# Performance work log

Measured on AMD Instinct MI355X. Metric: run time of the kernel, lower is better.

The kernel has to match this reference:

```python
import jax, jax.numpy as jnp
import numpy as np

N_NODES = 50000
N_EDGES = 800000
D = 128  # in_dim == hidden_dim


def setup_inputs() -> dict:
    key = jax.random.key(0)
    k1, k2, k3, k4 = jax.random.split(key, 4)
    x = jax.random.normal(k1, (N_NODES, D), dtype=jnp.float32)
    edge_index = jax.random.randint(k2, (2, N_EDGES), 0, N_NODES, dtype=jnp.int64)
    # Glorot-ish scale for square weights
    scale = 1.0 / np.sqrt(D)
    W1 = jax.random.normal(k3, (D, D), dtype=jnp.float32) * scale
    W2 = jax.random.normal(k4, (D, D), dtype=jnp.float32) * scale
    b1 = jnp.zeros((D,), dtype=jnp.float32)
    b2 = jnp.zeros((D,), dtype=jnp.float32)
    return {"x": x, "edge_index": edge_index, "W1": W1, "b1": b1, "W2": W2, "b2": b2}


def _gcn_layer(x, W, b, src, dst, norm, n):
    # PyG GCNConv: h = x @ W, then symmetric-normalized scatter-add, then + bias
    h = x @ W                                   # [N, D] dense GEMM
    msg = h[src] * norm[:, None]                # [E', D] gather + scale
    out = jax.ops.segment_sum(msg, dst, num_segments=n)  # scatter-add
    return out + b


def reference(x, edge_index, W1, b1, W2, b2):
    n = x.shape[0]
    # add self-loops (GCNConv default add_self_loops=True)
    loops = jnp.arange(n, dtype=edge_index.dtype)
    src = jnp.concatenate([edge_index[0], loops])
    dst = jnp.concatenate([edge_index[1], loops])
    # symmetric normalization: deg^{-1/2}[src] * deg^{-1/2}[dst]
    deg = jax.ops.segment_sum(jnp.ones_like(src, dtype=x.dtype), dst, num_segments=n)
    dinv = jax.lax.rsqrt(jnp.maximum(deg, 1.0))  # deg >= 1 due to self-loops
    norm = dinv[src] * dinv[dst]
    # layer 1: conv -> relu (dropout is identity in eval mode)
    h = jax.nn.relu(_gcn_layer(x, W1, b1, src, dst, norm, n))
    # layer 2 (cut='c2'): conv -> relu
    h = jax.nn.relu(_gcn_layer(h, W2, b2, src, dst, norm, n))
    return h
```

## Files before the change

### kernel.cpp

```cpp
#include <hip/hip_runtime.h>
#include <hip/hip_fp16.h>

#define NN 50000
#define NE 800000
#define DD 128
#define NSTRIP 3125
#define NB 196
#define CHUNK 4096
#define MAXB 6144

#define OF_LCNT  0
#define OF_LOFS  50176
#define OF_DINV  100352
#define OF_DEG   150352
#define OF_OFFS2 200352
#define OF_TMP2  300352
#define OF_CSRW  1103168
#define OF_H1    2307392
#define OF_H2    5507392
#define OF_W1H   8707392
#define OF_W1L   8715584
#define OF_W2H   8723776
#define OF_W2L   8731968

typedef __attribute__((ext_vector_type(8))) short bf8_t;
typedef __attribute__((ext_vector_type(8))) unsigned short us8;
typedef __attribute__((ext_vector_type(4))) float f32x4;

static __device__ __forceinline__ unsigned short f2bf(float f) {
    unsigned int u = __float_as_uint(f);
    unsigned int r = (u + 0x7fffu + ((u >> 16) & 1u)) >> 16;
    return (unsigned short)r;
}
static __device__ __forceinline__ float bf2f(unsigned short h) {
    return __uint_as_float(((unsigned int)h) << 16);
}

__global__ void k_wconv(const float* __restrict__ W1, const float* __restrict__ W2,
                        ushort* __restrict__ w1h, ushort* __restrict__ w1l,
                        ushort* __restrict__ w2h, ushort* __restrict__ w2l,
                        int* __restrict__ deg) {
    int gg = blockIdx.x * 256 + threadIdx.x;
    for (int i = gg; i < NN; i += 4096) deg[i] = 0;
    const float* W = (gg < 2048) ? W1 : W2;
    ushort* wh = (gg < 2048) ? w1h : w2h;
    ushort* wl = (gg < 2048) ? w1l : w2l;
    int g = gg & 2047;
    int ntile = g >> 8;
    int kk = (g >> 6) & 3;
    int lane = g & 63;
    int k0 = kk * 32 + ((lane >> 4) * 8);
    int col = ntile * 16 + (lane & 15);
#pragma unroll
    for (int j = 0; j < 8; ++j) {
        float w = W[(k0 + j) * DD + col];
        unsigned short h = f2bf(w);
        wh[(size_t)g * 8 + j] = h;
        wl[(size_t)g * 8 + j] = f2bf(w - bf2f(h));
    }
}

__global__ __launch_bounds__(256) void k_prep(
        const int* __restrict__ src, const int* __restrict__ dst,
        int* __restrict__ lcnt_g, int* __restrict__ lofs_g,
        unsigned int* __restrict__ tmp2, int* __restrict__ deg,
        const float* __restrict__ X,
        const ushort* __restrict__ wh, const ushort* __restrict__ wl,
        ushort* __restrict__ H1) {
    __shared__ int lcnt[256];
    __shared__ int lsc[256];
    __shared__ int lcur[256];
    int tid = threadIdx.x;
    if (blockIdx.x < 196) {
        int blk = blockIdx.x;
        lcnt[tid] = 0;
        __syncthreads();
        int e0 = blk * CHUNK;
        int e1 = e0 + CHUNK; if (e1 > NE) e1 = NE;
        for (int e = e0 + tid; e < e1; e += 256) {
            int d = dst[e];
            atomicAdd(&lcnt[d >> 8], 1);
            atomicAdd(&deg[d], 1);
        }
        __syncthreads();
        int v = lcnt[tid];
        lsc[tid] = v;
        __syncthreads();
        for (int o = 1; o < 256; o <<= 1) {
            int t = (tid >= o) ? lsc[tid - o] : 0;
            __syncthreads();
            lsc[tid] += t;
            __syncthreads();
        }
        int excl = lsc[tid] - v;
        lcnt_g[tid * 196 + blk] = v;
        lofs_g[tid * 196 + blk] = excl;
        lcur[tid] = excl;
        __syncthreads();
        for (int e = e0 + tid; e < e1; e += 256) {
            int d = dst[e], s = src[e];
            int b = d >> 8;
            int r = atomicAdd(&lcur[b], 1);
            tmp2[blk * CHUNK + r] = ((unsigned int)s << 8) | (unsigned int)(d & 255);
        }
        return;
    }
    int wave = tid >> 6;
    int lane = tid & 63;
    int strip = (blockIdx.x - 196) * 4 + wave;
    if (strip >= NSTRIP) return;
    int rb = strip << 4;
    int m = lane & 15;
    int quad = lane >> 4;
    const float* ar = X + (size_t)(rb + m) * DD;
    f32x4 acc[8];
#pragma unroll
    for (int t = 0; t < 8; ++t) acc[t] = (f32x4){0.f, 0.f, 0.f, 0.f};
#pragma unroll
    for (int kk = 0; kk < 4; ++kk) {
        float4 xa = *(const float4*)(ar + kk * 32 + quad * 8);
        float4 xb = *(const float4*)(ar + kk * 32 + quad * 8 + 4);
        float xs[8] = {xa.x, xa.y, xa.z, xa.w, xb.x, xb.y, xb.z, xb.w};
        bf8_t ah, al;
#pragma unroll
        for (int j = 0; j < 8; ++j) {
            unsigned short hh = f2bf(xs[j]);
            ah[j] = (short)hh;
            al[j] = (short)f2bf(xs[j] - bf2f(hh));
        }
#pragma unroll
        for (int t = 0; t < 8; ++t) {
            size_t bo = ((size_t)(t * 4 + kk) * 64 + lane) * 8;
            bf8_t bh = *(const bf8_t*)(wh + bo);
            bf8_t bl = *(const bf8_t*)(wl + bo);
            acc[t] = __builtin_amdgcn_mfma_f32_16x16x32_bf16(ah, bh, acc[t], 0, 0, 0);
            acc[t] = __builtin_amdgcn_mfma_f32_16x16x32_bf16(ah, bl, acc[t], 0, 0, 0);
            acc[t] = __builtin_amdgcn_mfma_f32_16x16x32_bf16(al, bh, acc[t], 0, 0, 0);
        }
    }
#pragma unroll
    for (int t = 0; t < 8; ++t) {
#pragma unroll
        for (int r = 0; r < 4; ++r)
            H1[(size_t)(rb + quad * 4 + r) * DD + t * 16 + m] = f2bf(acc[t][r]);
    }
}

__global__ __launch_bounds__(256) void k_sort(const int* __restrict__ lcnt_g,
                                              const int* __restrict__ lofs_g,
                                              const unsigned int* __restrict__ tmp2,
                                              const int* __restrict__ deg,
                                              unsigned int* __restrict__ csrw,
                                              int2* __restrict__ offs2,
                                              float* __restrict__ dinv) {
    __shared__ unsigned int ent[MAXB];
    __shared__ int c[256];
    __shared__ int p[256];
    __shared__ int o[256];
    __shared__ int cnt[256];
    __shared__ int boff[256];
    __shared__ int cur[256];
    __shared__ float sdv[256];
    int b = blockIdx.x, tid = threadIdx.x;
    int cv = (tid < 196) ? lcnt_g[b * 196 + tid] : 0;
    o[tid] = (tid < 196) ? lofs_g[b * 196 + tid] : 0;
    c[tid] = cv;
    p[tid] = cv;
    cnt[tid] = 0;
    __syncthreads();
    for (int s = 1; s < 256; s <<= 1) {
        int t = (tid >= s) ? p[tid - s] : 0;
        __syncthreads();
        p[tid] += t;
        __syncthreads();
    }
    int nb = p[255];
    for (int i = tid; i < nb; i += 256) {
        int lo = 0, hi = 255;
#pragma unroll
        for (int it = 0; it < 8; ++it) {
            int mid = (lo + hi) >> 1;
            if (p[mid] > i) hi = mid; else lo = mid + 1;
        }
        int blk = lo;
        int j = i - (p[blk] - c[blk]);
        unsigned int e = tmp2[blk * CHUNK + o[blk] + j];
        ent[i] = e;
        atomicAdd(&cnt[e & 255], 1);
    }
    __syncthreads();
    int v = cnt[tid];
    boff[tid] = v;
    __syncthreads();
    for (int s = 1; s < 256; s <<= 1) {
        int t = (tid >= s) ? boff[tid - s] : 0;
        __syncthreads();
        boff[tid] += t;
        __syncthreads();
    }
    int excl = boff[tid] - v;
    int base = b * MAXB;
    int node = b * 256 + tid;
    float dv = rsqrtf((float)(v + 1));
    sdv[tid] = dv;
    if (node < NN) {
        offs2[node] = make_int2(base + excl, base + excl + v);
        dinv[node] = dv;
    }
    cur[tid] = excl;
    __syncthreads();
    for (int i = tid; i < nb; i += 256) {
        unsigned int e = ent[i];
        int bin = e & 255;
        int s = (int)(e >> 8);
        int r = atomicAdd(&cur[bin], 1);
        float w = rsqrtf((float)(deg[s] + 1)) * sdv[bin];
        csrw[base + r] = ((unsigned int)s << 16) |
                         (unsigned int)__half_as_ushort(__float2half(w));
    }
}

__global__ __launch_bounds__(512) void k_aggmm(const ushort* __restrict__ h1,
                                               const float* __restrict__ dinv,
                                               const int2* __restrict__ offs2,
                                               const unsigned int* __restrict__ csrw,
                                               const float* __restrict__ b1,
                                               const ushort* __restrict__ w2h,
                                               const ushort* __restrict__ w2l,
                                               ushort* __restrict__ h2) {
    __shared__ float xs[16][136];
    int wave = threadIdx.x >> 6;
    int lane = threadIdx.x & 63;
    int rb = blockIdx.x * 16;
    int q = lane >> 4;
    int l = lane & 15;
    const float* bp = b1 + 8 * l;
    for (int nn = 0; nn < 2; ++nn) {
        int node = rb + wave * 2 + nn;
        int2 oe = offs2[node];
        int e1 = oe.y;
        float a[8] = {0.f, 0.f, 0.f, 0.f, 0.f, 0.f, 0.f, 0.f};
        for (int eb = oe.x; eb < e1; eb += 32) {
            int s[8]; float w[8];
#pragma unroll
            for (int j = 0; j < 8; ++j) {
                int e = eb + q + 4 * j;
                int er = (e < e1) ? e : (e1 - 1);
                er = (er < 0) ? 0 : er;
                unsigned int rw = csrw[er];
                s[j] = (int)(rw >> 16);
                w[j] = (e < e1)
                     ? __half2float(__ushort_as_half((unsigned short)(rw & 0xffffu)))
                     : 0.f;
            }
            us8 v[8];
#pragma unroll
            for (int j = 0; j < 8; ++j)
                v[j] = *(const us8*)(h1 + ((size_t)s[j] << 7) + 8 * l);
#pragma unroll
            for (int j = 0; j < 8; ++j) {
#pragma unroll
                for (int d = 0; d < 8; ++d) a[d] += w[j] * bf2f(v[j][d]);
            }
        }
        float dnode = dinv[node];
        if (q == 0) {
            us8 v = *(const us8*)(h1 + ((size_t)node << 7) + 8 * l);
            float ws = dnode * dnode;
#pragma unroll
            for (int j = 0; j < 8; ++j) a[j] += ws * bf2f(v[j]);
        }
#pragma unroll
        for (int j = 0; j < 8; ++j) {
            a[j] += __shfl_xor(a[j], 16, 64);
            a[j] += __shfl_xor(a[j], 32, 64);
        }
        if (q == 0) {
            float* xr = &xs[wave * 2 + nn][8 * l];
#pragma unroll
            for (int j = 0; j < 8; ++j)
                xr[j] = fmaxf(a[j] + bp[j], 0.f);
        }
    }
    __syncthreads();
    int m = lane & 15;
    int quad = lane >> 4;
    int t = wave;
    f32x4 acc = (f32x4){0.f, 0.f, 0.f, 0.f};
#pragma unroll
    for (int kk = 0; kk < 4; ++kk) {
        const float* xr = &xs[m][kk * 32 + quad * 8];
        float4 xa = *(const float4*)xr;
        float4 xb = *(const float4*)(xr + 4);
        float xv[8] = {xa.x, xa.y, xa.z, xa.w, xb.x, xb.y, xb.z, xb.w};
        bf8_t ah, al;
#pragma unroll
        for (int j = 0; j < 8; ++j) {
            unsigned short hh = f2bf(xv[j]);
            ah[j] = (short)hh;
            al[j] = (short)f2bf(xv[j] - bf2f(hh));
        }
        size_t bo = ((size_t)(t * 4 + kk) * 64 + lane) * 8;
        bf8_t bh = *(const bf8_t*)(w2h + bo);
        bf8_t bl = *(const bf8_t*)(w2l + bo);
        acc = __builtin_amdgcn_mfma_f32_16x16x32_bf16(ah, bh, acc, 0, 0, 0);
        acc = __builtin_amdgcn_mfma_f32_16x16x32_bf16(ah, bl, acc, 0, 0, 0);
        acc = __builtin_amdgcn_mfma_f32_16x16x32_bf16(al, bh, acc, 0, 0, 0);
    }
#pragma unroll
    for (int r = 0; r < 4; ++r)
        h2[(size_t)(rb + quad * 4 + r) * DD + t * 16 + m] = f2bf(acc[r]);
}

__global__ __launch_bounds__(256) void k_agg(const ushort* __restrict__ h,
                                             const float* __restrict__ dinv,
                                             const int2* __restrict__ offs2,
                                             const unsigned int* __restrict__ csrw,
                                             const float* __restrict__ bias,
                                             float* __restrict__ outf) {
    int wave = threadIdx.x >> 6;
    int lane = threadIdx.x & 63;
    int node = blockIdx.x * 4 + wave;
    int q = lane >> 4;
    int l = lane & 15;
    int2 oe = offs2[node];
    int e1 = oe.y;
    float a[8] = {0.f, 0.f, 0.f, 0.f, 0.f, 0.f, 0.f, 0.f};
    for (int eb = oe.x; eb < e1; eb += 32) {
        int s[8]; float w[8];
#pragma unroll
        for (int j = 0; j < 8; ++j) {
            int e = eb + q + 4 * j;
            int er = (e < e1) ? e : (e1 - 1);
            er = (er < 0) ? 0 : er;
            unsigned int rw = csrw[er];
            s[j] = (int)(rw >> 16);
            w[j] = (e < e1)
                 ? __half2float(__ushort_as_half((unsigned short)(rw & 0xffffu)))
                 : 0.f;
        }
        us8 v[8];
#pragma unroll
        for (int j = 0; j < 8; ++j)
            v[j] = *(const us8*)(h + ((size_t)s[j] << 7) + 8 * l);
#pragma unroll
        for (int j = 0; j < 8; ++j) {
#pragma unroll
            for (int d = 0; d < 8; ++d) a[d] += w[j] * bf2f(v[j][d]);
        }
    }
    float dnode = dinv[node];
    if (q == 0) {
        us8 v = *(const us8*)(h + ((size_t)node << 7) + 8 * l);
        float ws = dnode * dnode;
#pragma unroll
        for (int j = 0; j < 8; ++j) a[j] += ws * bf2f(v[j]);
    }
#pragma unroll
    for (int j = 0; j < 8; ++j) {
        a[j] += __shfl_xor(a[j], 16, 64);
        a[j] += __shfl_xor(a[j], 32, 64);
    }
    if (q == 0) {
        float* op = outf + (size_t)node * DD + 8 * l;
        const float* bp = bias + 8 * l;
        float4 o0, o1;
        o0.x = fmaxf(a[0] + bp[0], 0.f);
        o0.y = fmaxf(a[1] + bp[1], 0.f);
        o0.z = fmaxf(a[2] + bp[2], 0.f);
        o0.w = fmaxf(a[3] + bp[3], 0.f);
        o1.x = fmaxf(a[4] + bp[4], 0.f);
        o1.y = fmaxf(a[5] + bp[5], 0.f);
        o1.z = fmaxf(a[6] + bp[6], 0.f);
        o1.w = fmaxf(a[7] + bp[7], 0.f);
        *(float4*)op = o0;
        *(float4*)(op + 4) = o1;
    }
}

extern "C" void kernel_launch(void* const* d_in, const int* in_sizes, int n_in,
                              void* d_out, int out_size, void* d_ws, size_t ws_size,
                              hipStream_t stream) {
    const float* x  = (const float*)d_in[0];
    const int*   ei = (const int*)d_in[1];
    const float* W1 = (const float*)d_in[2];
    const float* b1 = (const float*)d_in[3];
    const float* W2 = (const float*)d_in[4];
    const float* b2 = (const float*)d_in[5];
    float* out = (float*)d_out;

    const int* src = ei;
    const int* dst = ei + NE;

    int*          wsi  = (int*)d_ws;
    float*        wsf  = (float*)d_ws;
    ushort*       wsu  = (ushort*)d_ws;
    unsigned int* wsuw = (unsigned int*)d_ws;
    int*    lcnt_g = wsi + OF_LCNT;
    int*    lofs_g = wsi + OF_LOFS;
    float*  dinv   = wsf + OF_DINV;
    int*    deg    = wsi + OF_DEG;
    int2*   offs2  = (int2*)(wsi + OF_OFFS2);
    unsigned int* tmp2 = wsuw + OF_TMP2;
    unsigned int* csrw = wsuw + OF_CSRW;
    ushort* h1     = wsu + (size_t)OF_H1 * 2;
    ushort* h2     = wsu + (size_t)OF_H2 * 2;
    ushort* w1h    = wsu + (size_t)OF_W1H * 2;
    ushort* w1l    = wsu + (size_t)OF_W1L * 2;
    ushort* w2h    = wsu + (size_t)OF_W2H * 2;
    ushort* w2l    = wsu + (size_t)OF_W2L * 2;

    hipLaunchKernelGGL(k_wconv, dim3(16), dim3(256), 0, stream,
                       W1, W2, w1h, w1l, w2h, w2l, deg);
    hipLaunchKernelGGL(k_prep, dim3(196 + (NSTRIP + 3) / 4), dim3(256), 0, stream,
                       src, dst, lcnt_g, lofs_g, tmp2, deg, x, w1h, w1l, h1);
    hipLaunchKernelGGL(k_sort, dim3(NB), dim3(256), 0, stream,
                       lcnt_g, lofs_g, tmp2, deg, csrw, offs2, dinv);
    hipLaunchKernelGGL(k_aggmm, dim3(NSTRIP), dim3(512), 0, stream,
                       h1, dinv, offs2, csrw, b1, w2h, w2l, h2);
    hipLaunchKernelGGL(k_agg, dim3(NN / 4), dim3(256), 0, stream,
                       h2, dinv, offs2, csrw, b2, out);
}
```

Before: 226.7 us.

## Drop per-edge weights and global degree atomics; merge prep kernels into two launches

Removes the global degree atomic counter and the per-edge fp16 weight packing. CSR entries are now 16-bit source indices only, and aggregation fetches dinv[src] per edge and applies dinv[dst] once after summation. Weight conversion is merged with bucketing, and the first GEMM is merged with the sort kernel, going from five launches to four. The cost is an extra random dinv gather per edge during both aggregations, in exchange for less global atomic traffic, half-size CSR entries and one fewer launch.

Measured after the change: 220.3 us. 1.03x faster.

```diff
diff --git a/kernel.cpp b/kernel.cpp
--- a/kernel.cpp
+++ b/kernel.cpp
@@ -1,5 +1,4 @@
 #include <hip/hip_runtime.h>
-#include <hip/hip_fp16.h>
 
 #define NN 50000
 #define NE 800000
@@ -12,16 +11,15 @@
 #define OF_LCNT  0
 #define OF_LOFS  50176
 #define OF_DINV  100352
-#define OF_DEG   150352
-#define OF_OFFS2 200352
-#define OF_TMP2  300352
-#define OF_CSRW  1103168
-#define OF_H1    2307392
-#define OF_H2    5507392
-#define OF_W1H   8707392
-#define OF_W1L   8715584
-#define OF_W2H   8723776
-#define OF_W2L   8731968
+#define OF_OFFS2 150352
+#define OF_TMP2  250352
+#define OF_CSRU  1053168
+#define OF_H1    1655280
+#define OF_H2    4855280
+#define OF_W1H   8055280
+#define OF_W1L   8063472
+#define OF_W2H   8071664
+#define OF_W2L   8079856
 
 typedef __attribute__((ext_vector_type(8))) short bf8_t;
 typedef __attribute__((ext_vector_type(8))) unsigned short us8;
@@ -36,72 +34,135 @@
     return __uint_as_float(((unsigned int)h) << 16);
 }
 
-__global__ void k_wconv(const float* __restrict__ W1, const float* __restrict__ W2,
-                        ushort* __restrict__ w1h, ushort* __restrict__ w1l,
-                        ushort* __restrict__ w2h, ushort* __restrict__ w2l,
-                        int* __restrict__ deg) {
-    int gg = blockIdx.x * 256 + threadIdx.x;
-    for (int i = gg; i < NN; i += 4096) deg[i] = 0;
-    const float* W = (gg < 2048) ? W1 : W2;
-    ushort* wh = (gg < 2048) ? w1h : w2h;
-    ushort* wl = (gg < 2048) ? w1l : w2l;
-    int g = gg & 2047;
-    int ntile = g >> 8;
-    int kk = (g >> 6) & 3;
-    int lane = g & 63;
-    int k0 = kk * 32 + ((lane >> 4) * 8);
-    int col = ntile * 16 + (lane & 15);
-#pragma unroll
-    for (int j = 0; j < 8; ++j) {
-        float w = W[(k0 + j) * DD + col];
-        unsigned short h = f2bf(w);
-        wh[(size_t)g * 8 + j] = h;
-        wl[(size_t)g * 8 + j] = f2bf(w - bf2f(h));
-    }
-}
-
-__global__ __launch_bounds__(256) void k_prep(
+__global__ __launch_bounds__(256) void k_ws(
+        const float* __restrict__ W1, const float* __restrict__ W2,
+        ushort* __restrict__ w1h, ushort* __restrict__ w1l,
+        ushort* __restrict__ w2h, ushort* __restrict__ w2l,
         const int* __restrict__ src, const int* __restrict__ dst,
         int* __restrict__ lcnt_g, int* __restrict__ lofs_g,
-        unsigned int* __restrict__ tmp2, int* __restrict__ deg,
-        const float* __restrict__ X,
-        const ushort* __restrict__ wh, const ushort* __restrict__ wl,
-        ushort* __restrict__ H1) {
+        unsigned int* __restrict__ tmp2) {
     __shared__ int lcnt[256];
     __shared__ int lsc[256];
     __shared__ int lcur[256];
     int tid = threadIdx.x;
+    if (blockIdx.x < 16) {
+        int gg = blockIdx.x * 256 + tid;
+        const float* W = (gg < 2048) ? W1 : W2;
+        ushort* wh = (gg < 2048) ? w1h : w2h;
+        ushort* wl = (gg < 2048) ? w1l : w2l;
+        int g = gg & 2047;
+        int ntile = g >> 8;
+        int kk = (g >> 6) & 3;
+        int lane = g & 63;
+        int k0 = kk * 32 + ((lane >> 4) * 8);
+        int col = ntile * 16 + (lane & 15);
+#pragma unroll
+        for (int j = 0; j < 8; ++j) {
+            float w = W[(k0 + j) * DD + col];
+            unsigned short h = f2bf(w);
+            wh[(size_t)g * 8 + j] = h;
+            wl[(size_t)g * 8 + j] = f2bf(w - bf2f(h));
+        }
+        return;
+    }
+    int blk = blockIdx.x - 16;
+    lcnt[tid] = 0;
+    __syncthreads();
+    int e0 = blk * CHUNK;
+    int e1 = e0 + CHUNK; if (e1 > NE) e1 = NE;
+    for (int e = e0 + tid; e < e1; e += 256)
+        atomicAdd(&lcnt[dst[e] >> 8], 1);
+    __syncthreads();
+    int v = lcnt[tid];
+    lsc[tid] = v;
+    __syncthreads();
+    for (int o = 1; o < 256; o <<= 1) {
+        int t = (tid >= o) ? lsc[tid - o] : 0;
+        __syncthreads();
+        lsc[tid] += t;
+        __syncthreads();
+    }
+    int excl = lsc[tid] - v;
+    lcnt_g[tid * 196 + blk] = v;
+    lofs_g[tid * 196 + blk] = excl;
+    lcur[tid] = excl;
+    __syncthreads();
+    for (int e = e0 + tid; e < e1; e += 256) {
+        int d = dst[e], s = src[e];
+        int b = d >> 8;
+        int r = atomicAdd(&lcur[b], 1);
+        tmp2[blk * CHUNK + r] = ((unsigned int)s << 8) | (unsigned int)(d & 255);
+    }
+}
+
+__global__ __launch_bounds__(256) void k_sg(
+        const int* __restrict__ lcnt_g, const int* __restrict__ lofs_g,
+        const unsigned int* __restrict__ tmp2,
+        ushort* __restrict__ csru, int2* __restrict__ offs2,
+        float* __restrict__ dinv,
+        const float* __restrict__ X,
+        const ushort* __restrict__ wh, const ushort* __restrict__ wl,
+        ushort* __restrict__ H1) {
+    __shared__ unsigned int ent[MAXB];
+    __shared__ int c[256];
+    __shared__ int p[256];
+    __shared__ int o[256];
+    __shared__ int cnt[256];
+    __shared__ int boff[256];
+    __shared__ int cur[256];
+    int tid = threadIdx.x;
     if (blockIdx.x < 196) {
-        int blk = blockIdx.x;
-        lcnt[tid] = 0;
-        __syncthreads();
-        int e0 = blk * CHUNK;
-        int e1 = e0 + CHUNK; if (e1 > NE) e1 = NE;
-        for (int e = e0 + tid; e < e1; e += 256) {
-            int d = dst[e];
-            atomicAdd(&lcnt[d >> 8], 1);
-            atomicAdd(&deg[d], 1);
-        }
-        __syncthreads();
-        int v = lcnt[tid];
-        lsc[tid] = v;
-        __syncthreads();
-        for (int o = 1; o < 256; o <<= 1) {
-            int t = (tid >= o) ? lsc[tid - o] : 0;
+        int b = blockIdx.x;
+        int cv = (tid < 196) ? lcnt_g[b * 196 + tid] : 0;
+        o[tid] = (tid < 196) ? lofs_g[b * 196 + tid] : 0;
+        c[tid] = cv;
+        p[tid] = cv;
+        cnt[tid] = 0;
+        __syncthreads();
+        for (int s = 1; s < 256; s <<= 1) {
+            int t = (tid >= s) ? p[tid - s] : 0;
             __syncthreads();
-            lsc[tid] += t;
+            p[tid] += t;
             __syncthreads();
         }
-        int excl = lsc[tid] - v;
-        lcnt_g[tid * 196 + blk] = v;
-        lofs_g[tid * 196 + blk] = excl;
-        lcur[tid] = excl;
-        __syncthreads();
-        for (int e = e0 + tid; e < e1; e += 256) {
-            int d = dst[e], s = src[e];
-            int b = d >> 8;
-            int r = atomicAdd(&lcur[b], 1);
-            tmp2[blk * CHUNK + r] = ((unsigned int)s << 8) | (unsigned int)(d & 255);
+        int nb = p[255];
+        for (int i = tid; i < nb; i += 256) {
+            int lo = 0, hi = 255;
+#pragma unroll
+            for (int it = 0; it < 8; ++it) {
+                int mid = (lo + hi) >> 1;
+                if (p[mid] > i) hi = mid; else lo = mid + 1;
+            }
+            int blk = lo;
+            int j = i - (p[blk] - c[blk]);
+            unsigned int e = tmp2[blk * CHUNK + o[blk] + j];
+            ent[i] = e;
+            atomicAdd(&cnt[e & 255], 1);
+        }
+        __syncthreads();
+        int v = cnt[tid];
+        boff[tid] = v;
+        __syncthreads();
+        for (int s = 1; s < 256; s <<= 1) {
+            int t = (tid >= s) ? boff[tid - s] : 0;
+            __syncthreads();
+            boff[tid] += t;
+            __syncthreads();
+        }
+        int excl = boff[tid] - v;
+        int base = b * MAXB;
+        int node = b * 256 + tid;
+        if (node < NN) {
+            offs2[node] = make_int2(base + excl, base + excl + v);
+            dinv[node] = rsqrtf((float)(v + 1));
+        }
+        cur[tid] = excl;
+        __syncthreads();
+        for (int i = tid; i < nb; i += 256) {
+            unsigned int e = ent[i];
+            int bin = e & 255;
+            int r = atomicAdd(&cur[bin], 1);
+            csru[base + r] = (ushort)(e >> 8);
         }
         return;
     }
@@ -146,84 +207,10 @@
     }
 }
 
-__global__ __launch_bounds__(256) void k_sort(const int* __restrict__ lcnt_g,
-                                              const int* __restrict__ lofs_g,
-                                              const unsigned int* __restrict__ tmp2,
-                                              const int* __restrict__ deg,
-                                              unsigned int* __restrict__ csrw,
-                                              int2* __restrict__ offs2,
-                                              float* __restrict__ dinv) {
-    __shared__ unsigned int ent[MAXB];
-    __shared__ int c[256];
-    __shared__ int p[256];
-    __shared__ int o[256];
-    __shared__ int cnt[256];
-    __shared__ int boff[256];
-    __shared__ int cur[256];
-    __shared__ float sdv[256];
-    int b = blockIdx.x, tid = threadIdx.x;
-    int cv = (tid < 196) ? lcnt_g[b * 196 + tid] : 0;
-    o[tid] = (tid < 196) ? lofs_g[b * 196 + tid] : 0;
-    c[tid] = cv;
-    p[tid] = cv;
-    cnt[tid] = 0;
-    __syncthreads();
-    for (int s = 1; s < 256; s <<= 1) {
-        int t = (tid >= s) ? p[tid - s] : 0;
-        __syncthreads();
-        p[tid] += t;
-        __syncthreads();
-    }
-    int nb = p[255];
-    for (int i = tid; i < nb; i += 256) {
-        int lo = 0, hi = 255;
-#pragma unroll
-        for (int it = 0; it < 8; ++it) {
-            int mid = (lo + hi) >> 1;
-            if (p[mid] > i) hi = mid; else lo = mid + 1;
-        }
-        int blk = lo;
-        int j = i - (p[blk] - c[blk]);
-        unsigned int e = tmp2[blk * CHUNK + o[blk] + j];
-        ent[i] = e;
-        atomicAdd(&cnt[e & 255], 1);
-    }
-    __syncthreads();
-    int v = cnt[tid];
-    boff[tid] = v;
-    __syncthreads();
-    for (int s = 1; s < 256; s <<= 1) {
-        int t = (tid >= s) ? boff[tid - s] : 0;
-        __syncthreads();
-        boff[tid] += t;
-        __syncthreads();
-    }
-    int excl = boff[tid] - v;
-    int base = b * MAXB;
-    int node = b * 256 + tid;
-    float dv = rsqrtf((float)(v + 1));
-    sdv[tid] = dv;
-    if (node < NN) {
-        offs2[node] = make_int2(base + excl, base + excl + v);
-        dinv[node] = dv;
-    }
-    cur[tid] = excl;
-    __syncthreads();
-    for (int i = tid; i < nb; i += 256) {
-        unsigned int e = ent[i];
-        int bin = e & 255;
-        int s = (int)(e >> 8);
-        int r = atomicAdd(&cur[bin], 1);
-        float w = rsqrtf((float)(deg[s] + 1)) * sdv[bin];
-        csrw[base + r] = ((unsigned int)s << 16) |
-                         (unsigned int)__half_as_ushort(__float2half(w));
-    }
-}
-
 __global__ __launch_bounds__(512) void k_aggmm(const ushort* __restrict__ h1,
                                                const float* __restrict__ dinv,
                                                const int2* __restrict__ offs2,
-                                               const unsigned int* __restrict__ csrw,
+                                               const ushort* __restrict__ csru,
                                                const float* __restrict__ b1,
                                                const ushort* __restrict__ w2h,
                                                const ushort* __restrict__ w2l,
@@ -247,11 +234,8 @@
                 int e = eb + q + 4 * j;
                 int er = (e < e1) ? e : (e1 - 1);
                 er = (er < 0) ? 0 : er;
-                unsigned int rw = csrw[er];
-                s[j] = (int)(rw >> 16);
-                w[j] = (e < e1)
-                     ? __half2float(__ushort_as_half((unsigned short)(rw & 0xffffu)))
-                     : 0.f;
+                s[j] = (int)csru[er];
+                w[j] = (e < e1) ? dinv[s[j]] : 0.f;
             }
             us8 v[8];
 #pragma unroll
@@ -266,9 +250,8 @@
         float dnode = dinv[node];
         if (q == 0) {
             us8 v = *(const us8*)(h1 + ((size_t)node << 7) + 8 * l);
-            float ws = dnode * dnode;
-#pragma unroll
-            for (int j = 0; j < 8; ++j) a[j] += ws * bf2f(v[j]);
+#pragma unroll
+            for (int j = 0; j < 8; ++j) a[j] += dnode * bf2f(v[j]);
         }
 #pragma unroll
         for (int j = 0; j < 8; ++j) {
@@ -279,7 +262,7 @@
             float* xr = &xs[wave * 2 + nn][8 * l];
 #pragma unroll
             for (int j = 0; j < 8; ++j)
-                xr[j] = fmaxf(a[j] + bp[j], 0.f);
+                xr[j] = fmaxf(dnode * a[j] + bp[j], 0.f);
         }
     }
     __syncthreads();
@@ -315,7 +298,7 @@
 __global__ __launch_bounds__(256) void k_agg(const ushort* __restrict__ h,
                                              const float* __restrict__ dinv,
                                              const int2* __restrict__ offs2,
-                                             const unsigned int* __restrict__ csrw,
+                                             const ushort* __restrict__ csru,
                                              const float* __restrict__ bias,
                                              float* __restrict__ outf) {
     int wave = threadIdx.x >> 6;
@@ -333,11 +316,8 @@
             int e = eb + q + 4 * j;
             int er = (e < e1) ? e : (e1 - 1);
             er = (er < 0) ? 0 : er;
-            unsigned int rw = csrw[er];
-            s[j] = (int)(rw >> 16);
-            w[j] = (e < e1)
-                 ? __half2float(__ushort_as_half((unsigned short)(rw & 0xffffu)))
-                 : 0.f;
+            s[j] = (int)csru[er];
+            w[j] = (e < e1) ? dinv[s[j]] : 0.f;
         }
         us8 v[8];
 #pragma unroll
@@ -352,9 +332,8 @@
     float dnode = dinv[node];
     if (q == 0) {
         us8 v = *(const us8*)(h + ((size_t)node << 7) + 8 * l);
-        float ws = dnode * dnode;
-#pragma unroll
-        for (int j = 0; j < 8; ++j) a[j] += ws * bf2f(v[j]);
+#pragma unroll
+        for (int j = 0; j < 8; ++j) a[j] += dnode * bf2f(v[j]);
     }
 #pragma unroll
     for (int j = 0; j < 8; ++j) {
@@ -365,14 +344,14 @@
         float* op = outf + (size_t)node * DD + 8 * l;
         const float* bp = bias + 8 * l;
         float4 o0, o1;
-        o0.x = fmaxf(a[0] + bp[0], 0.f);
-        o0.y = fmaxf(a[1] + bp[1], 0.f);
-        o0.z = fmaxf(a[2] + bp[2], 0.f);
-        o0.w = fmaxf(a[3] + bp[3], 0.f);
-        o1.x = fmaxf(a[4] + bp[4], 0.f);
-        o1.y = fmaxf(a[5] + bp[5], 0.f);
-        o1.z = fmaxf(a[6] + bp[6], 0.f);
-        o1.w = fmaxf(a[7] + bp[7], 0.f);
+        o0.x = fmaxf(dnode * a[0] + bp[0], 0.f);
+        o0.y = fmaxf(dnode * a[1] + bp[1], 0.f);
+        o0.z = fmaxf(dnode * a[2] + bp[2], 0.f);
+        o0.w = fmaxf(dnode * a[3] + bp[3], 0.f);
+        o1.x = fmaxf(dnode * a[4] + bp[4], 0.f);
+        o1.y = fmaxf(dnode * a[5] + bp[5], 0.f);
+        o1.z = fmaxf(dnode * a[6] + bp[6], 0.f);
+        o1.w = fmaxf(dnode * a[7] + bp[7], 0.f);
         *(float4*)op = o0;
         *(float4*)(op + 4) = o1;
     }
@@ -399,10 +378,9 @@
     int*    lcnt_g = wsi + OF_LCNT;
     int*    lofs_g = wsi + OF_LOFS;
     float*  dinv   = wsf + OF_DINV;
-    int*    deg    = wsi + OF_DEG;
     int2*   offs2  = (int2*)(wsi + OF_OFFS2);
     unsigned int* tmp2 = wsuw + OF_TMP2;
-    unsigned int* csrw = wsuw + OF_CSRW;
+    ushort* csru   = wsu + (size_t)OF_CSRU * 2;
     ushort* h1     = wsu + (size_t)OF_H1 * 2;
     ushort* h2     = wsu + (size_t)OF_H2 * 2;
     ushort* w1h    = wsu + (size_t)OF_W1H * 2;
@@ -410,14 +388,14 @@
     ushort* w2h    = wsu + (size_t)OF_W2H * 2;
     ushort* w2l    = wsu + (size_t)OF_W2L * 2;
 
-    hipLaunchKernelGGL(k_wconv, dim3(16), dim3(256), 0, stream,
-                       W1, W2, w1h, w1l, w2h, w2l, deg);
-    hipLaunchKernelGGL(k_prep, dim3(196 + (NSTRIP + 3) / 4), dim3(256), 0, stream,
-                       src, dst, lcnt_g, lofs_g, tmp2, deg, x, w1h, w1l, h1);
-    hipLaunchKernelGGL(k_sort, dim3(NB), dim3(256), 0, stream,
-                       lcnt_g, lofs_g, tmp2, deg, csrw, offs2, dinv);
+    hipLaunchKernelGGL(k_ws, dim3(16 + 196), dim3(256), 0, stream,
+                       W1, W2, w1h, w1l, w2h, w2l,
+                       src, dst, lcnt_g, lofs_g, tmp2);
+    hipLaunchKernelGGL(k_sg, dim3(196 + (NSTRIP + 3) / 4), dim3(256), 0, stream,
+                       lcnt_g, lofs_g, tmp2, csru, offs2, dinv,
+                       x, w1h, w1l, h1);
     hipLaunchKernelGGL(k_aggmm, dim3(NSTRIP), dim3(512), 0, stream,
-                       h1, dinv, offs2, csrw, b1, w2h, w2l, h2);
+                       h1, dinv, offs2, csru, b1, w2h, w2l, h2);
     hipLaunchKernelGGL(k_agg, dim3(NN / 4), dim3(256), 0, stream,
-                       h2, dinv, offs2, csrw, b2, out);
-}
+                       h2, dinv, offs2, csru, b2, out);
+}
```
